# Kernel optimization log

Measured on AMD Instinct MI355X. Metric: run time of the kernel, lower is better.

## Reference

```python
import jax, jax.numpy as jnp
import numpy as np
import math

B, S, D, H = 4, 2048, 1024, 16
DEPTH = D // H


def setup_inputs() -> dict:
    key = jax.random.key(0)
    ks = jax.random.split(key, 8)
    scale = 1.0 / math.sqrt(D)
    return {
        "v": jax.random.normal(ks[0], (B, S, D), dtype=jnp.float32),
        "k": jax.random.normal(ks[1], (B, S, D), dtype=jnp.float32),
        "q": jax.random.normal(ks[2], (B, S, D), dtype=jnp.float32),
        "wq_w": jax.random.normal(ks[3], (D, D), dtype=jnp.float32) * scale,
        "wq_b": jnp.zeros((D,), dtype=jnp.float32),
        "wk_w": jax.random.normal(ks[4], (D, D), dtype=jnp.float32) * scale,
        "wk_b": jnp.zeros((D,), dtype=jnp.float32),
        "wv_w": jax.random.normal(ks[5], (D, D), dtype=jnp.float32) * scale,
        "wv_b": jnp.zeros((D,), dtype=jnp.float32),
        "dense_w": jax.random.normal(ks[6], (D, D), dtype=jnp.float32) * scale,
        "dense_b": jnp.zeros((D,), dtype=jnp.float32),
    }


def _split_heads(x):
    # [B, S, D] -> [B, H, S, depth]
    b, s, _ = x.shape
    return x.reshape(b, s, H, DEPTH).transpose(0, 2, 1, 3)


def reference(v, k, q, wq_w, wq_b, wk_w, wk_b, wv_w, wv_b, dense_w, dense_b):
    # Linear projections (torch Linear: x @ W.T + b)
    qh = _split_heads(q @ wq_w.T + wq_b)
    kh = _split_heads(k @ wk_w.T + wk_b)
    vh = _split_heads(v @ wv_w.T + wv_b)

    # scaled dot-product attention; scores: [B, H, S, S]
    scores = jnp.einsum("bhqd,bhkd->bhqk", qh, kh) / math.sqrt(DEPTH)
    attn = jax.nn.softmax(scores, axis=-1)
    ctx = jnp.einsum("bhqk,bhkd->bhqd", attn, vh)

    # merge heads: [B, H, S, depth] -> [B, S, D]
    ctx = ctx.transpose(0, 2, 1, 3).reshape(q.shape[0], -1, D)
    return ctx @ dense_w.T + dense_b
```

## Files before the change

kernel.cpp:

```cpp
#include <hip/hip_runtime.h>
#include <hip/hip_bf16.h>
#include <stdint.h>

#define B_  4
#define S_  2048
#define D_  1024
#define H_  16
#define DP_ 64
#define M_  (B_*S_)

typedef __bf16 bf16x8 __attribute__((ext_vector_type(8)));
typedef float  f32x4  __attribute__((ext_vector_type(4)));
typedef unsigned short u16x8 __attribute__((ext_vector_type(8)));

__device__ __forceinline__ unsigned short f2bf(float f) {
    unsigned u = __builtin_bit_cast(unsigned, f);
    u += 0x7fffu + ((u >> 16) & 1u);
    return (unsigned short)(u >> 16);
}
__device__ __forceinline__ unsigned pk_bf16(float lo, float hi) {
    unsigned a = __builtin_bit_cast(unsigned, lo);
    unsigned b = __builtin_bit_cast(unsigned, hi);
    a += 0x7fffu + ((a >> 16) & 1u);
    b += 0x7fffu + ((b >> 16) & 1u);
    return __builtin_amdgcn_perm(b, a, 0x07060302u);
}
__device__ __forceinline__ bf16x8 ld_frag(const unsigned short* p) {
    return __builtin_bit_cast(bf16x8, *(const u16x8*)p);
}
__device__ __forceinline__ f32x4 mfma16(bf16x8 a, bf16x8 b, f32x4 c) {
    return __builtin_amdgcn_mfma_f32_16x16x32_bf16(a, b, c, 0, 0, 0);
}
__device__ __forceinline__ void gl2lds16(const void* g, void* l) {
    __builtin_amdgcn_global_load_lds(
        (const __attribute__((address_space(1))) unsigned*)g,
        (__attribute__((address_space(3))) unsigned*)l, 16, 0, 0);
}

__global__ __launch_bounds__(256)
void cvt_all(const float* __restrict__ w0, const float* __restrict__ w1,
             const float* __restrict__ w2, const float* __restrict__ w3,
             const float* __restrict__ a0, const float* __restrict__ a1,
             const float* __restrict__ a2,
             unsigned short* __restrict__ Wcat, unsigned short* __restrict__ Acat)
{
    const int gid = blockIdx.x * 256 + threadIdx.x;
    const float* src; unsigned short* dst;
    if (gid < 524288) {
        const int wi = gid >> 17;
        const size_t off = (size_t)(gid & 131071) * 8;
        const float* ws[4] = {w0, w1, w2, w3};
        src = ws[wi] + off; dst = Wcat + (size_t)wi * 1048576 + off;
    } else {
        const int g2 = gid - 524288;
        const int ai = g2 >> 20;
        const size_t off = (size_t)(g2 & 1048575) * 8;
        const float* as[3] = {a0, a1, a2};
        src = as[ai] + off; dst = Acat + (size_t)ai * 8388608 + off;
    }
    float4 x = ((const float4*)src)[0];
    float4 y = ((const float4*)src)[1];
    uint4 o;
    o.x = pk_bf16(x.x, x.y); o.y = pk_bf16(x.z, x.w);
    o.z = pk_bf16(y.x, y.y); o.w = pk_bf16(y.z, y.w);
    *(uint4*)dst = o;
}

template<bool OUT_HEADS>
__global__ __launch_bounds__(256, 4)
void gemm_bt(const unsigned short* __restrict__ Acat, size_t a_stride,
             const unsigned short* __restrict__ Wcat,
             const float* __restrict__ bias0, const float* __restrict__ bias1,
             const float* __restrict__ bias2, void* __restrict__ Out)
{
    __shared__ __align__(16) unsigned short As[128 * 32];
    __shared__ __align__(16) unsigned short Bs[128 * 32];

    const int z = blockIdx.z;
    const unsigned short* A = Acat + (size_t)z * a_stride;
    const unsigned short* W = Wcat + ((size_t)z << 20);
    const float* bias = (z == 0) ? bias0 : ((z == 1) ? bias1 : bias2);
    const float scale = (OUT_HEADS && z == 0) ? 0.125f : 1.0f;

    const int tid  = threadIdx.x;
    const int wave = tid >> 6, lane = tid & 63;
    const int quad = lane >> 4, l16 = lane & 15;
    const int wm = (wave >> 1) * 64, wn = (wave & 1) * 64;
    const int row0 = blockIdx.x * 128, col0 = blockIdx.y * 128;

    const int crow = lane >> 2;
    const int cg   = (lane & 3) ^ (crow & 3);

    f32x4 acc[4][4];
#pragma unroll
    for (int i = 0; i < 4; i++)
#pragma unroll
        for (int j = 0; j < 4; j++) acc[i][j] = (f32x4){0.f, 0.f, 0.f, 0.f};

    auto stage = [&](int kt) {
        const int k0 = kt * 32;
#pragma unroll
        for (int j = 0; j < 2; ++j) {
            const int c = wave * 2 + j;
            gl2lds16(A + (size_t)(row0 + c * 16 + crow) * D_ + k0 + cg * 8,
                     (unsigned char*)As + c * 1024);
            gl2lds16(W + (size_t)(col0 + c * 16 + crow) * D_ + k0 + cg * 8,
                     (unsigned char*)Bs + c * 1024);
        }
    };

    stage(0);
    for (int kt = 0; kt < D_ / 32; ++kt) {
        __syncthreads();
        bf16x8 af[4], bv[4];
#pragma unroll
        for (int mi = 0; mi < 4; ++mi) {
            const int row = wm + mi * 16 + l16;
            af[mi] = ld_frag(&As[row * 32 + ((quad ^ (row & 3)) * 8)]);
        }
#pragma unroll
        for (int ni = 0; ni < 4; ++ni) {
            const int row = wn + ni * 16 + l16;
            bv[ni] = ld_frag(&Bs[row * 32 + ((quad ^ (row & 3)) * 8)]);
        }
        if (kt + 1 < D_ / 32) {
            __syncthreads();
            stage(kt + 1);
        }
#pragma unroll
        for (int mi = 0; mi < 4; ++mi)
#pragma unroll
            for (int ni = 0; ni < 4; ++ni)
                acc[mi][ni] = mfma16(af[mi], bv[ni], acc[mi][ni]);
    }

#pragma unroll
    for (int ni = 0; ni < 4; ni++) {
        const int col = col0 + wn + ni * 16 + l16;
        const float bvv = bias[col];
#pragma unroll
        for (int mi = 0; mi < 4; mi++) {
            const int rowb = row0 + wm + mi * 16 + quad * 4;
#pragma unroll
            for (int r = 0; r < 4; r++) {
                const int row = rowb + r;
                float vv = acc[mi][ni][r] + bvv;
                if (OUT_HEADS) {
                    vv *= scale;
                    const int b = row >> 11, s = row & (S_ - 1);
                    const int h = col >> 6,  dp = col & (DP_ - 1);
                    ((unsigned short*)Out)[(size_t)z * 8388608 +
                        (((size_t)(b * H_ + h) * S_ + s) * DP_) + dp] = f2bf(vv);
                } else {
                    ((float*)Out)[(size_t)row * D_ + col] = vv;
                }
            }
        }
    }
}

__global__ __launch_bounds__(256)
void flash_attn(const unsigned short* __restrict__ Qh,
                const unsigned short* __restrict__ Kh,
                const unsigned short* __restrict__ Vh,
                unsigned short* __restrict__ Ctx)
{
    constexpr int LP = 40;
    __shared__ __align__(16) unsigned short Kt[128 * 64];
    __shared__ __align__(16) unsigned       Vt32[64 * 64];

    const int tid  = threadIdx.x;
    const int wave = tid >> 6, lane = tid & 63;
    const int quad = lane >> 4, l16 = lane & 15;
    const int bh = blockIdx.x, qt = blockIdx.y;
    const size_t base = (size_t)bh * S_ * DP_;

    bf16x8 qf[2][2];
#pragma unroll
    for (int mi = 0; mi < 2; mi++)
#pragma unroll
        for (int kd = 0; kd < 2; kd++)
            qf[mi][kd] = ld_frag(&Qh[base + (size_t)(qt * 128 + wave * 32 + mi * 16 + l16) * DP_ + kd * 32 + quad * 8]);

    f32x4 o[2][4];
    float mst[2], lst[2];
#pragma unroll
    for (int mi = 0; mi < 2; mi++) {
#pragma unroll
        for (int nd = 0; nd < 4; nd++) o[mi][nd] = (f32x4){0.f, 0.f, 0.f, 0.f};
        mst[mi] = -1e30f; lst[mi] = 0.f;
    }

    unsigned short* pw = Kt + wave * 32 * LP;
    const float c_log2e = 1.44269504f;
    const int kswz = ((lane & 7) ^ (lane >> 3)) * 8;

    for (int t = 0; t < S_ / 128; ++t) {
        __syncthreads();
        {
#pragma unroll
            for (int j = 0; j < 4; ++j) {
                const int c = wave * 4 + j;
                gl2lds16(Kh + base + (size_t)(t * 128 + c * 8 + (lane >> 3)) * DP_ + kswz,
                         Kt + c * 512);
            }
        }
        {
            const unsigned short* g = Vh + base + (size_t)(t * 128 + lane * 2) * DP_ + wave * 16;
            unsigned short va[16], vb[16];
            *(uint4*)&va[0] = *(const uint4*)g;         *(uint4*)&va[8] = *(const uint4*)(g + 8);
            *(uint4*)&vb[0] = *(const uint4*)(g + DP_); *(uint4*)&vb[8] = *(const uint4*)(g + DP_ + 8);
#pragma unroll
            for (int i = 0; i < 16; ++i)
                Vt32[(wave * 16 + i) * 64 + (((lane >> 2) ^ i) * 4) + (lane & 3)] =
                    (unsigned)va[i] | ((unsigned)vb[i] << 16);
        }
        __syncthreads();

        f32x4 st[8][2];
#pragma unroll
        for (int kb = 0; kb < 8; ++kb) { st[kb][0] = (f32x4){0,0,0,0}; st[kb][1] = (f32x4){0,0,0,0}; }
#pragma unroll
        for (int kb = 0; kb < 8; ++kb) {
            const int krow = (kb * 16 + l16) * 64;
            bf16x8 kf0 = ld_frag(&Kt[krow + (((quad)     ^ (l16 & 7)) * 8)]);
            bf16x8 kf1 = ld_frag(&Kt[krow + (((4 + quad) ^ (l16 & 7)) * 8)]);
            st[kb][0] = mfma16(kf0, qf[0][0], st[kb][0]);
            st[kb][0] = mfma16(kf1, qf[0][1], st[kb][0]);
            st[kb][1] = mfma16(kf0, qf[1][0], st[kb][1]);
            st[kb][1] = mfma16(kf1, qf[1][1], st[kb][1]);
        }

        float alpha[2];
#pragma unroll
        for (int mi = 0; mi < 2; ++mi) {
            float mx = -1e30f;
#pragma unroll
            for (int kb = 0; kb < 8; ++kb)
#pragma unroll
                for (int r = 0; r < 4; ++r) mx = fmaxf(mx, st[kb][mi][r]);
            mx = fmaxf(mx, __shfl_xor(mx, 16, 64));
            mx = fmaxf(mx, __shfl_xor(mx, 32, 64));
            const float mnew = fmaxf(mst[mi], mx);
            const float mb = mnew * c_log2e;
            float sum = 0.f;
#pragma unroll
            for (int kb = 0; kb < 8; ++kb)
#pragma unroll
                for (int r = 0; r < 4; ++r) {
                    float p = __builtin_amdgcn_exp2f(st[kb][mi][r] * c_log2e - mb);
                    st[kb][mi][r] = p;
                    sum += p;
                }
            sum += __shfl_xor(sum, 16, 64);
            sum += __shfl_xor(sum, 32, 64);
            alpha[mi] = __builtin_amdgcn_exp2f(mst[mi] * c_log2e - mb);
            lst[mi] = lst[mi] * alpha[mi] + sum;
            mst[mi] = mnew;
        }
#pragma unroll
        for (int mi = 0; mi < 2; ++mi)
#pragma unroll
            for (int r = 0; r < 4; ++r) {
                float aT = __shfl(alpha[mi], quad * 4 + r, 64);
#pragma unroll
                for (int nd = 0; nd < 4; ++nd) o[mi][nd][r] *= aT;
            }

        __syncthreads();

#pragma unroll
        for (int ch = 0; ch < 4; ++ch) {
#pragma unroll
            for (int kk = 0; kk < 2; ++kk)
#pragma unroll
                for (int mi = 0; mi < 2; ++mi) {
                    f32x4 p = st[2 * ch + kk][mi];
                    uint2 w;
                    w.x = pk_bf16(p[0], p[1]);
                    w.y = pk_bf16(p[2], p[3]);
                    *(uint2*)&pw[(mi * 16 + l16) * LP + kk * 16 + quad * 4] = w;
                }
            asm volatile("s_waitcnt lgkmcnt(0)" ::: "memory");
            bf16x8 pa0 = ld_frag(&pw[(l16)      * LP + quad * 8]);
            bf16x8 pa1 = ld_frag(&pw[(16 + l16) * LP + quad * 8]);
#pragma unroll
            for (int nd = 0; nd < 4; ++nd) {
                bf16x8 vbf = ld_frag((const unsigned short*)
                    &Vt32[(nd * 16 + l16) * 64 + (((ch * 4 + quad) ^ l16) * 4)]);
                o[0][nd] = mfma16(pa0, vbf, o[0][nd]);
                o[1][nd] = mfma16(pa1, vbf, o[1][nd]);
            }
            asm volatile("" ::: "memory");
        }
    }

    const int b = bh >> 4, h = bh & 15;
#pragma unroll
    for (int mi = 0; mi < 2; ++mi)
#pragma unroll
        for (int r = 0; r < 4; ++r) {
            const float lT  = __shfl(lst[mi], quad * 4 + r, 64);
            const float inv = __builtin_amdgcn_rcpf(lT);
            const int srw = qt * 128 + wave * 32 + mi * 16 + quad * 4 + r;
#pragma unroll
            for (int nd = 0; nd < 4; ++nd)
                Ctx[((size_t)(b * S_ + srw)) * D_ + h * DP_ + nd * 16 + l16] = f2bf(o[mi][nd][r] * inv);
        }
}

extern "C" void kernel_launch(void* const* d_in, const int* in_sizes, int n_in,
                              void* d_out, int out_size, void* d_ws, size_t ws_size,
                              hipStream_t stream)
{
    const float* v    = (const float*)d_in[0];
    const float* k    = (const float*)d_in[1];
    const float* q    = (const float*)d_in[2];
    const float* wq_w = (const float*)d_in[3];
    const float* wq_b = (const float*)d_in[4];
    const float* wk_w = (const float*)d_in[5];
    const float* wk_b = (const float*)d_in[6];
    const float* wv_w = (const float*)d_in[7];
    const float* wv_b = (const float*)d_in[8];
    const float* dw   = (const float*)d_in[9];
    const float* db   = (const float*)d_in[10];
    float* out = (float*)d_out;

    unsigned short* Qh   = (unsigned short*)d_ws;
    unsigned short* Kh   = Qh   + (size_t)M_ * D_;
    unsigned short* Vh   = Kh   + (size_t)M_ * D_;
    unsigned short* Ctx  = Vh   + (size_t)M_ * D_;
    unsigned short* Wcat = Ctx  + (size_t)M_ * D_;
    unsigned short* Acat = Wcat + (size_t)4 * D_ * D_;

    cvt_all<<<14336, 256, 0, stream>>>(wq_w, wk_w, wv_w, dw, q, k, v, Wcat, Acat);

    dim3 blk(256);
    gemm_bt<true><<<dim3(M_ / 128, D_ / 128, 3), blk, 0, stream>>>(
        Acat, (size_t)M_ * D_, Wcat, wq_b, wk_b, wv_b, Qh);

    flash_attn<<<dim3(B_ * H_, S_ / 128), blk, 0, stream>>>(Qh, Kh, Vh, Ctx);

    gemm_bt<false><<<dim3(M_ / 128, D_ / 128, 1), blk, 0, stream>>>(
        Ctx, 0, Wcat + (size_t)3 * D_ * D_, db, db, db, out);
}
```

Before: 389.0 us.

## Emit V pre-transposed from projection GEMM and widen GEMM K-tile to 64

The QKV projection GEMM now writes V in a transposed [B,H,depth,S] layout through an LDS staging pass, so the attention kernel can load V tiles with direct global-to-LDS copies instead of transposing V per tile with register shuffles and scalar LDS stores. The GEMM also moves from a 32-wide to a 64-wide K tile with a new XOR swizzle, which halves the number of barrier-separated iterations but doubles LDS use and lowers the occupancy hint from 4 to 3 blocks. The V epilogue adds extra barriers and an LDS round trip in the projection kernel.

```diff
diff --git a/kernel.cpp b/kernel.cpp
--- a/kernel.cpp
+++ b/kernel.cpp
@@ -67,20 +67,20 @@
 }
 
 template<bool OUT_HEADS>
-__global__ __launch_bounds__(256, 4)
+__global__ __launch_bounds__(256, 3)
 void gemm_bt(const unsigned short* __restrict__ Acat, size_t a_stride,
              const unsigned short* __restrict__ Wcat,
              const float* __restrict__ bias0, const float* __restrict__ bias1,
              const float* __restrict__ bias2, void* __restrict__ Out)
 {
-    __shared__ __align__(16) unsigned short As[128 * 32];
-    __shared__ __align__(16) unsigned short Bs[128 * 32];
+    __shared__ __align__(16) unsigned short SM[16384];
+    unsigned short* As = SM;
+    unsigned short* Bs = SM + 8192;
 
     const int z = blockIdx.z;
     const unsigned short* A = Acat + (size_t)z * a_stride;
     const unsigned short* W = Wcat + ((size_t)z << 20);
     const float* bias = (z == 0) ? bias0 : ((z == 1) ? bias1 : bias2);
-    const float scale = (OUT_HEADS && z == 0) ? 0.125f : 1.0f;
 
     const int tid  = threadIdx.x;
     const int wave = tid >> 6, lane = tid & 63;
@@ -88,8 +88,8 @@
     const int wm = (wave >> 1) * 64, wn = (wave & 1) * 64;
     const int row0 = blockIdx.x * 128, col0 = blockIdx.y * 128;
 
-    const int crow = lane >> 2;
-    const int cg   = (lane & 3) ^ (crow & 3);
+    const int srow = lane >> 3;
+    const int sg   = (lane & 7) ^ srow;
 
     f32x4 acc[4][4];
 #pragma unroll
@@ -98,62 +98,111 @@
         for (int j = 0; j < 4; j++) acc[i][j] = (f32x4){0.f, 0.f, 0.f, 0.f};
 
     auto stage = [&](int kt) {
-        const int k0 = kt * 32;
-#pragma unroll
-        for (int j = 0; j < 2; ++j) {
-            const int c = wave * 2 + j;
-            gl2lds16(A + (size_t)(row0 + c * 16 + crow) * D_ + k0 + cg * 8,
+        const int k0 = kt * 64;
+#pragma unroll
+        for (int j = 0; j < 4; ++j) {
+            const int c = wave * 4 + j;
+            gl2lds16(A + (size_t)(row0 + c * 8 + srow) * D_ + k0 + sg * 8,
                      (unsigned char*)As + c * 1024);
-            gl2lds16(W + (size_t)(col0 + c * 16 + crow) * D_ + k0 + cg * 8,
+            gl2lds16(W + (size_t)(col0 + c * 8 + srow) * D_ + k0 + sg * 8,
                      (unsigned char*)Bs + c * 1024);
         }
     };
 
     stage(0);
-    for (int kt = 0; kt < D_ / 32; ++kt) {
+    for (int kt = 0; kt < D_ / 64; ++kt) {
         __syncthreads();
-        bf16x8 af[4], bv[4];
+        bf16x8 af[4][2], bv[4][2];
 #pragma unroll
         for (int mi = 0; mi < 4; ++mi) {
             const int row = wm + mi * 16 + l16;
-            af[mi] = ld_frag(&As[row * 32 + ((quad ^ (row & 3)) * 8)]);
+#pragma unroll
+            for (int kd = 0; kd < 2; ++kd)
+                af[mi][kd] = ld_frag(&As[row * 64 + (((kd * 4 + quad) ^ (row & 7)) * 8)]);
         }
 #pragma unroll
         for (int ni = 0; ni < 4; ++ni) {
             const int row = wn + ni * 16 + l16;
-            bv[ni] = ld_frag(&Bs[row * 32 + ((quad ^ (row & 3)) * 8)]);
-        }
-        if (kt + 1 < D_ / 32) {
+#pragma unroll
+            for (int kd = 0; kd < 2; ++kd)
+                bv[ni][kd] = ld_frag(&Bs[row * 64 + (((kd * 4 + quad) ^ (row & 7)) * 8)]);
+        }
+        if (kt + 1 < D_ / 64) {
             __syncthreads();
             stage(kt + 1);
         }
 #pragma unroll
-        for (int mi = 0; mi < 4; ++mi)
-#pragma unroll
-            for (int ni = 0; ni < 4; ++ni)
-                acc[mi][ni] = mfma16(af[mi], bv[ni], acc[mi][ni]);
-    }
-
-#pragma unroll
-    for (int ni = 0; ni < 4; ni++) {
-        const int col = col0 + wn + ni * 16 + l16;
-        const float bvv = bias[col];
-#pragma unroll
-        for (int mi = 0; mi < 4; mi++) {
-            const int rowb = row0 + wm + mi * 16 + quad * 4;
-#pragma unroll
-            for (int r = 0; r < 4; r++) {
-                const int row = rowb + r;
-                float vv = acc[mi][ni][r] + bvv;
-                if (OUT_HEADS) {
-                    vv *= scale;
+        for (int kd = 0; kd < 2; ++kd)
+#pragma unroll
+            for (int mi = 0; mi < 4; ++mi)
+#pragma unroll
+                for (int ni = 0; ni < 4; ++ni)
+                    acc[mi][ni] = mfma16(af[mi][kd], bv[ni][kd], acc[mi][ni]);
+    }
+
+    if constexpr (OUT_HEADS) {
+        if (z == 2) {
+            unsigned short* Lt = SM;
+            unsigned short* OutV = (unsigned short*)Out + (size_t)2 * 8388608;
+            const int bidx = row0 >> 11;
+#pragma unroll
+            for (int hc = 0; hc < 2; ++hc) {
+                __syncthreads();
+                if ((wave & 1) == hc) {
+#pragma unroll
+                    for (int ni = 0; ni < 4; ++ni) {
+                        const float bvv = bias[col0 + hc * 64 + ni * 16 + l16];
+#pragma unroll
+                        for (int mi = 0; mi < 4; ++mi) {
+                            uint2 w;
+                            w.x = pk_bf16(acc[mi][ni][0] + bvv, acc[mi][ni][1] + bvv);
+                            w.y = pk_bf16(acc[mi][ni][2] + bvv, acc[mi][ni][3] + bvv);
+                            *(uint2*)&Lt[(ni * 16 + l16) * 132 + wm + mi * 16 + quad * 4] = w;
+                        }
+                    }
+                }
+                __syncthreads();
+                const int hg = (col0 >> 6) + hc;
+                const size_t vb = ((size_t)(bidx * H_ + hg) * DP_) * S_;
+#pragma unroll
+                for (int p = 0; p < 4; ++p) {
+                    const int dpl = p * 16 + (tid >> 4);
+                    uint4 d = *(const uint4*)&Lt[dpl * 132 + (tid & 15) * 8];
+                    *(uint4*)(OutV + vb + (size_t)dpl * S_ + (row0 & (S_ - 1)) + (tid & 15) * 8) = d;
+                }
+            }
+            return;
+        }
+        const float scale = (z == 0) ? 0.125f : 1.0f;
+#pragma unroll
+        for (int ni = 0; ni < 4; ni++) {
+            const int col = col0 + wn + ni * 16 + l16;
+            const float bvv = bias[col];
+            const int h = col >> 6, dp = col & (DP_ - 1);
+#pragma unroll
+            for (int mi = 0; mi < 4; mi++) {
+                const int rowb = row0 + wm + mi * 16 + quad * 4;
+#pragma unroll
+                for (int r = 0; r < 4; r++) {
+                    const int row = rowb + r;
                     const int b = row >> 11, s = row & (S_ - 1);
-                    const int h = col >> 6,  dp = col & (DP_ - 1);
                     ((unsigned short*)Out)[(size_t)z * 8388608 +
-                        (((size_t)(b * H_ + h) * S_ + s) * DP_) + dp] = f2bf(vv);
-                } else {
-                    ((float*)Out)[(size_t)row * D_ + col] = vv;
-                }
+                        (((size_t)(b * H_ + h) * S_ + s) * DP_) + dp] =
+                        f2bf((acc[mi][ni][r] + bvv) * scale);
+                }
+            }
+        }
+    } else {
+#pragma unroll
+        for (int ni = 0; ni < 4; ni++) {
+            const int col = col0 + wn + ni * 16 + l16;
+            const float bvv = bias[col];
+#pragma unroll
+            for (int mi = 0; mi < 4; mi++) {
+                const int rowb = row0 + wm + mi * 16 + quad * 4;
+#pragma unroll
+                for (int r = 0; r < 4; r++)
+                    ((float*)Out)[(size_t)(rowb + r) * D_ + col] = acc[mi][ni][r] + bvv;
             }
         }
     }
@@ -162,12 +211,12 @@
 __global__ __launch_bounds__(256)
 void flash_attn(const unsigned short* __restrict__ Qh,
                 const unsigned short* __restrict__ Kh,
-                const unsigned short* __restrict__ Vh,
+                const unsigned short* __restrict__ Vtg,
                 unsigned short* __restrict__ Ctx)
 {
     constexpr int LP = 40;
     __shared__ __align__(16) unsigned short Kt[128 * 64];
-    __shared__ __align__(16) unsigned       Vt32[64 * 64];
+    __shared__ __align__(16) unsigned short Vt[64 * 128];
 
     const int tid  = threadIdx.x;
     const int wave = tid >> 6, lane = tid & 63;
@@ -194,26 +243,19 @@
     unsigned short* pw = Kt + wave * 32 * LP;
     const float c_log2e = 1.44269504f;
     const int kswz = ((lane & 7) ^ (lane >> 3)) * 8;
+    const int vdp_l = lane >> 4;
+    const int vslot = lane & 15;
 
     for (int t = 0; t < S_ / 128; ++t) {
         __syncthreads();
-        {
-#pragma unroll
-            for (int j = 0; j < 4; ++j) {
-                const int c = wave * 4 + j;
-                gl2lds16(Kh + base + (size_t)(t * 128 + c * 8 + (lane >> 3)) * DP_ + kswz,
-                         Kt + c * 512);
-            }
-        }
-        {
-            const unsigned short* g = Vh + base + (size_t)(t * 128 + lane * 2) * DP_ + wave * 16;
-            unsigned short va[16], vb[16];
-            *(uint4*)&va[0] = *(const uint4*)g;         *(uint4*)&va[8] = *(const uint4*)(g + 8);
-            *(uint4*)&vb[0] = *(const uint4*)(g + DP_); *(uint4*)&vb[8] = *(const uint4*)(g + DP_ + 8);
-#pragma unroll
-            for (int i = 0; i < 16; ++i)
-                Vt32[(wave * 16 + i) * 64 + (((lane >> 2) ^ i) * 4) + (lane & 3)] =
-                    (unsigned)va[i] | ((unsigned)vb[i] << 16);
+#pragma unroll
+        for (int j = 0; j < 4; ++j) {
+            const int ck = wave * 4 + j;
+            gl2lds16(Kh + base + (size_t)(t * 128 + ck * 8 + (lane >> 3)) * DP_ + kswz,
+                     (unsigned char*)Kt + ck * 1024);
+            const int dp = ck * 4 + vdp_l;
+            gl2lds16(Vtg + base + (size_t)dp * S_ + t * 128 + ((vslot ^ (dp & 15)) * 8),
+                     (unsigned char*)Vt + ck * 1024);
         }
         __syncthreads();
 
@@ -286,8 +328,8 @@
             bf16x8 pa1 = ld_frag(&pw[(16 + l16) * LP + quad * 8]);
 #pragma unroll
             for (int nd = 0; nd < 4; ++nd) {
-                bf16x8 vbf = ld_frag((const unsigned short*)
-                    &Vt32[(nd * 16 + l16) * 64 + (((ch * 4 + quad) ^ l16) * 4)]);
+                const int dp = nd * 16 + l16;
+                bf16x8 vbf = ld_frag(&Vt[dp * 128 + (((ch * 4 + quad) ^ l16) * 8)]);
                 o[0][nd] = mfma16(pa0, vbf, o[0][nd]);
                 o[1][nd] = mfma16(pa1, vbf, o[1][nd]);
             }
@@ -328,8 +370,8 @@
 
     unsigned short* Qh   = (unsigned short*)d_ws;
     unsigned short* Kh   = Qh   + (size_t)M_ * D_;
-    unsigned short* Vh   = Kh   + (size_t)M_ * D_;
-    unsigned short* Ctx  = Vh   + (size_t)M_ * D_;
+    unsigned short* Vt   = Kh   + (size_t)M_ * D_;
+    unsigned short* Ctx  = Vt   + (size_t)M_ * D_;
     unsigned short* Wcat = Ctx  + (size_t)M_ * D_;
     unsigned short* Acat = Wcat + (size_t)4 * D_ * D_;
 
@@ -339,7 +381,7 @@
     gemm_bt<true><<<dim3(M_ / 128, D_ / 128, 3), blk, 0, stream>>>(
         Acat, (size_t)M_ * D_, Wcat, wq_b, wk_b, wv_b, Qh);
 
-    flash_attn<<<dim3(B_ * H_, S_ / 128), blk, 0, stream>>>(Qh, Kh, Vh, Ctx);
+    flash_attn<<<dim3(B_ * H_, S_ / 128), blk, 0, stream>>>(Qh, Kh, Vt, Ctx);
 
     gemm_bt<false><<<dim3(M_ / 128, D_ / 128, 1), blk, 0, stream>>>(
         Ctx, 0, Wcat + (size_t)3 * D_ * D_, db, db, db, out);
```

New measurement: 383.1 us. No clear change (-1.5%).
